# Kernel tuning notes

Measured on AMD Instinct MI355X. Metric: run time of the kernel, lower is better.

## Reference

```python
import jax, jax.numpy as jnp
import numpy as np

N_NODES = 40000
FEAT = 128
HID = 128
EMB = 64
N_EDGES = 640000


def setup_inputs() -> dict:
    key = jax.random.key(0)
    ks = jax.random.split(key, 8)
    x = jax.random.normal(ks[0], (N_NODES, FEAT), dtype=jnp.float32)
    edge_index = jax.random.randint(ks[1], (2, N_EDGES), 0, N_NODES, dtype=jnp.int64)
    s1 = 1.0 / np.sqrt(FEAT)
    s2 = 1.0 / np.sqrt(HID)
    W1_l = jax.random.uniform(ks[2], (HID, FEAT), jnp.float32, -s1, s1)
    b1 = jax.random.uniform(ks[3], (HID,), jnp.float32, -s1, s1)
    W1_r = jax.random.uniform(ks[4], (HID, FEAT), jnp.float32, -s1, s1)
    W2_l = jax.random.uniform(ks[5], (EMB, HID), jnp.float32, -s2, s2)
    b2 = jax.random.uniform(ks[6], (EMB,), jnp.float32, -s2, s2)
    W2_r = jax.random.uniform(ks[7], (EMB, HID), jnp.float32, -s2, s2)
    return {"x": x, "edge_index": edge_index, "W1_l": W1_l, "b1": b1,
            "W1_r": W1_r, "W2_l": W2_l, "b2": b2, "W2_r": W2_r}


def _sage_conv(x, src, dst, W_l, b_l, W_r, n_nodes):
    # mean aggregation of source-node features onto destination nodes
    msg = x[src]                                           # [E, d]
    agg = jax.ops.segment_sum(msg, dst, num_segments=n_nodes)   # [N, d]
    cnt = jax.ops.segment_sum(jnp.ones((src.shape[0],), x.dtype), dst,
                              num_segments=n_nodes)        # [N]
    agg = agg / jnp.maximum(cnt, 1.0)[:, None]
    # out = lin_l(mean_j x_j) + lin_r(x_i); bias lives in lin_l
    return agg @ W_l.T + b_l + x @ W_r.T


def reference(x, edge_index, W1_l, b1, W1_r, W2_l, b2, W2_r):
    src, dst = edge_index[0], edge_index[1]
    n = x.shape[0]
    h = _sage_conv(x, src, dst, W1_l, b1, W1_r, n)
    h = jax.nn.elu(h)
    # dropout p=0.2 is identity in eval mode
    h = _sage_conv(h, src, dst, W2_l, b2, W2_r, n)
    return jax.nn.log_softmax(h, axis=1)
```

## Files before the change

kernel.cpp:

```cpp
#include <hip/hip_runtime.h>
#include <hip/hip_fp16.h>
#include <math.h>

#define N_NODES 40000
#define FEATD 128
#define EMB 64
#define N_EDGES 640000
#define CAP 64

typedef unsigned short u16;
typedef __attribute__((ext_vector_type(8))) unsigned short u16x8;
typedef __attribute__((ext_vector_type(8))) _Float16 f16x8;
typedef __attribute__((ext_vector_type(4))) float f32x4;

__device__ __forceinline__ float h2f(u16 h) {
  __half hh;
  *(u16*)&hh = h;
  return __half2float(hh);
}
__device__ __forceinline__ u16 f2h(float f) {
  __half hh = __float2half(f);
  return *(u16*)&hh;
}

__global__ __launch_bounds__(256) void prep_kernel(
    const float* __restrict__ x, const float* __restrict__ W1l,
    const float* __restrict__ W1r, const float* __restrict__ W2l,
    const float* __restrict__ W2r, u16* __restrict__ xh,
    u16* __restrict__ wp) {
  int bid = blockIdx.x;
  if (bid < 2500) {
    int i = bid * 256 + threadIdx.x;
    float4 v0 = *(const float4*)(&x[i * 8]);
    float4 v1 = *(const float4*)(&x[i * 8 + 4]);
    u16x8 o;
    o[0] = f2h(v0.x); o[1] = f2h(v0.y); o[2] = f2h(v0.z); o[3] = f2h(v0.w);
    o[4] = f2h(v1.x); o[5] = f2h(v1.y); o[6] = f2h(v1.z); o[7] = f2h(v1.w);
    *(u16x8*)(&xh[i * 8]) = o;
  } else {
    int i = (bid - 2500) * 256 + threadIdx.x;
    const float* srcp;
    int off;
    if (i < 16384)      { srcp = W1l; off = i; }
    else if (i < 32768) { srcp = W1r; off = i - 16384; }
    else if (i < 40960) { srcp = W2l; off = i - 32768; }
    else                { srcp = W2r; off = i - 40960; }
    wp[i] = f2h(srcp[off]);
  }
}

__global__ __launch_bounds__(256) void fill_kernel(
    const int* __restrict__ src, const int* __restrict__ dst,
    int* __restrict__ deg, u16* __restrict__ bucket) {
  int e = blockIdx.x * 256 + threadIdx.x;
  if (e >= N_EDGES) return;
  int s = src[e];
  int d = dst[e];
  int pos = atomicAdd(&deg[d], 1);
  if (pos < CAP) bucket[d * CAP + pos] = (u16)s;
}

__global__ __launch_bounds__(256) void gather_mean_f16(
    const u16* __restrict__ xh, const int* __restrict__ deg,
    const u16* __restrict__ bucket, u16* __restrict__ aggh) {
  int n = blockIdx.x * 4 + (threadIdx.x >> 6);
  int lane = threadIdx.x & 63;
  int g = lane >> 4;
  int li = lane & 15;
  int dgf = deg[n];
  int dg = dgf < CAP ? dgf : CAP;
  float inv = 1.0f / fmaxf((float)dgf, 1.0f);
  const u16* bk = bucket + n * CAP;
  float acc[8];
#pragma unroll
  for (int i = 0; i < 8; i++) acc[i] = 0.f;
  for (int d = g; d < dg; d += 4) {
    u16x8 v = *(const u16x8*)(&xh[(int)bk[d] * 128 + li * 8]);
#pragma unroll
    for (int i = 0; i < 8; i++) acc[i] += h2f(v[i]);
  }
#pragma unroll
  for (int i = 0; i < 8; i++) {
    acc[i] += __shfl_xor(acc[i], 16);
    acc[i] += __shfl_xor(acc[i], 32);
  }
  if (g == 0) {
    u16x8 o;
#pragma unroll
    for (int i = 0; i < 8; i++) o[i] = f2h(acc[i] * inv);
    *(u16x8*)(&aggh[n * 128 + li * 8]) = o;
  }
}

__global__ __launch_bounds__(256) void gemm12_kernel(
    const u16* __restrict__ AggH, const u16* __restrict__ XH,
    const u16* __restrict__ wp, const float* __restrict__ b1v,
    const float* __restrict__ b2v, u16* __restrict__ Yh,
    float* __restrict__ Z) {
  const u16* w1l = wp;
  const u16* w1r = wp + 16384;
  const u16* w2l = wp + 32768;
  const u16* w2r = wp + 40960;

  __shared__ __align__(16) union {
    struct {
      u16 wl[128][72], wr[128][72];
      u16 a[64][72], x[64][72];
    } p1;
    struct {
      u16 h[64][136];
      u16 w2l[64][136], w2r[64][136];
    } p2;
  } L;

  const int tid = threadIdx.x;
  const int wv = tid >> 6;
  const int lane = tid & 63;
  const int li = lane & 15;
  const int q = lane >> 4;
  const int nbase = blockIdx.x * 64;

  f32x4 acc1[8];
#pragma unroll
  for (int jt = 0; jt < 8; jt++) acc1[jt] = (f32x4){0.f, 0.f, 0.f, 0.f};

  for (int kb = 0; kb < 2; kb++) {
#pragma unroll
    for (int it = 0; it < 4; it++) {
      int idx = tid + 256 * it;
      int j = idx >> 3, c = idx & 7;
      int go = j * 128 + kb * 64 + c * 8;
      *(u16x8*)(&L.p1.wl[j][c * 8]) = *(const u16x8*)(&w1l[go]);
      *(u16x8*)(&L.p1.wr[j][c * 8]) = *(const u16x8*)(&w1r[go]);
    }
#pragma unroll
    for (int it = 0; it < 2; it++) {
      int idx = tid + 256 * it;
      int n = idx >> 3, c = idx & 7;
      int go = (nbase + n) * 128 + kb * 64 + c * 8;
      *(u16x8*)(&L.p1.a[n][c * 8]) = *(const u16x8*)(&AggH[go]);
      *(u16x8*)(&L.p1.x[n][c * 8]) = *(const u16x8*)(&XH[go]);
    }
    __syncthreads();
#pragma unroll
    for (int kk = 0; kk < 2; kk++) {
      f16x8 aF = *(const f16x8*)(&L.p1.a[wv * 16 + li][kk * 32 + q * 8]);
      f16x8 xF = *(const f16x8*)(&L.p1.x[wv * 16 + li][kk * 32 + q * 8]);
#pragma unroll
      for (int jt = 0; jt < 8; jt++) {
        f16x8 wlF = *(const f16x8*)(&L.p1.wl[jt * 16 + li][kk * 32 + q * 8]);
        f16x8 wrF = *(const f16x8*)(&L.p1.wr[jt * 16 + li][kk * 32 + q * 8]);
        acc1[jt] = __builtin_amdgcn_mfma_f32_16x16x32_f16(aF, wlF, acc1[jt], 0, 0, 0);
        acc1[jt] = __builtin_amdgcn_mfma_f32_16x16x32_f16(xF, wrF, acc1[jt], 0, 0, 0);
      }
    }
    __syncthreads();
  }

#pragma unroll
  for (int jt = 0; jt < 8; jt++) {
    int j = jt * 16 + li;
    float bb = b1v[j];
#pragma unroll
    for (int r = 0; r < 4; r++) {
      float v = acc1[jt][r] + bb;
      v = v > 0.f ? v : expm1f(v);
      L.p2.h[wv * 16 + q * 4 + r][j] = f2h(v);
    }
  }
#pragma unroll
  for (int it = 0; it < 4; it++) {
    int idx = tid + 256 * it;
    int j = idx >> 4, c = idx & 15;
    int go = j * 128 + c * 8;
    *(u16x8*)(&L.p2.w2l[j][c * 8]) = *(const u16x8*)(&w2l[go]);
    *(u16x8*)(&L.p2.w2r[j][c * 8]) = *(const u16x8*)(&w2r[go]);
  }
  __syncthreads();

  f32x4 accY[4], accZ[4];
#pragma unroll
  for (int mt = 0; mt < 4; mt++) {
    accY[mt] = (f32x4){0.f, 0.f, 0.f, 0.f};
    accZ[mt] = (f32x4){0.f, 0.f, 0.f, 0.f};
  }
#pragma unroll
  for (int kc = 0; kc < 4; kc++) {
    f16x8 blF = *(const f16x8*)(&L.p2.w2l[wv * 16 + li][kc * 32 + q * 8]);
    f16x8 brF = *(const f16x8*)(&L.p2.w2r[wv * 16 + li][kc * 32 + q * 8]);
#pragma unroll
    for (int mt = 0; mt < 4; mt++) {
      f16x8 hF = *(const f16x8*)(&L.p2.h[mt * 16 + li][kc * 32 + q * 8]);
      accY[mt] = __builtin_amdgcn_mfma_f32_16x16x32_f16(hF, blF, accY[mt], 0, 0, 0);
      accZ[mt] = __builtin_amdgcn_mfma_f32_16x16x32_f16(hF, brF, accZ[mt], 0, 0, 0);
    }
  }

  {
    int j2 = wv * 16 + li;
    float bb = b2v[j2];
#pragma unroll
    for (int mt = 0; mt < 4; mt++) {
#pragma unroll
      for (int r = 0; r < 4; r++) {
        int node = nbase + mt * 16 + q * 4 + r;
        Yh[node * 64 + j2] = f2h(accY[mt][r]);
        Z[node * 64 + j2] = accZ[mt][r] + bb;
      }
    }
  }
}

__global__ __launch_bounds__(256) void final_kernel(
    const u16* __restrict__ Y, const float* __restrict__ Z,
    const int* __restrict__ deg, const u16* __restrict__ bucket,
    float* __restrict__ out) {
  int n = blockIdx.x * 4 + (threadIdx.x >> 6);
  int lane = threadIdx.x & 63;
  int g = lane >> 4;
  int li = lane & 15;
  int dgf = deg[n];
  int dg = dgf < CAP ? dgf : CAP;
  float inv = 1.0f / fmaxf((float)dgf, 1.0f);
  const u16* bk = bucket + n * CAP;
  float4 acc = {0.f, 0.f, 0.f, 0.f};
  for (int d = g; d < dg; d += 4) {
    ushort4 v = *(const ushort4*)(&Y[(int)bk[d] * 64 + li * 4]);
    acc.x += h2f(v.x); acc.y += h2f(v.y); acc.z += h2f(v.z); acc.w += h2f(v.w);
  }
  acc.x += __shfl_xor(acc.x, 16); acc.y += __shfl_xor(acc.y, 16);
  acc.z += __shfl_xor(acc.z, 16); acc.w += __shfl_xor(acc.w, 16);
  acc.x += __shfl_xor(acc.x, 32); acc.y += __shfl_xor(acc.y, 32);
  acc.z += __shfl_xor(acc.z, 32); acc.w += __shfl_xor(acc.w, 32);
  float4 zb = *(const float4*)(&Z[n * 64 + li * 4]);
  float4 v;
  v.x = zb.x + acc.x * inv; v.y = zb.y + acc.y * inv;
  v.z = zb.z + acc.z * inv; v.w = zb.w + acc.w * inv;
  float m = fmaxf(fmaxf(v.x, v.y), fmaxf(v.z, v.w));
  m = fmaxf(m, __shfl_xor(m, 1)); m = fmaxf(m, __shfl_xor(m, 2));
  m = fmaxf(m, __shfl_xor(m, 4)); m = fmaxf(m, __shfl_xor(m, 8));
  float s = __expf(v.x - m) + __expf(v.y - m) + __expf(v.z - m) + __expf(v.w - m);
  s += __shfl_xor(s, 1); s += __shfl_xor(s, 2);
  s += __shfl_xor(s, 4); s += __shfl_xor(s, 8);
  float lg = m + logf(s);
  if (lane < 16) {
    float4 o = {v.x - lg, v.y - lg, v.z - lg, v.w - lg};
    *(float4*)(&out[n * 64 + li * 4]) = o;
  }
}

extern "C" void kernel_launch(void* const* d_in, const int* in_sizes, int n_in,
                              void* d_out, int out_size, void* d_ws, size_t ws_size,
                              hipStream_t stream) {
  const float* x   = (const float*)d_in[0];
  const int*   ei  = (const int*)d_in[1];
  const float* W1l = (const float*)d_in[2];
  const float* b1  = (const float*)d_in[3];
  const float* W1r = (const float*)d_in[4];
  const float* W2l = (const float*)d_in[5];
  const float* b2  = (const float*)d_in[6];
  const float* W2r = (const float*)d_in[7];
  float* out = (float*)d_out;

  const int* src = ei;
  const int* dst = ei + N_EDGES;

  u16* bucket = (u16*)d_ws;
  int* deg = (int*)(bucket + (size_t)N_NODES * CAP);
  u16* xh = (u16*)(deg + N_NODES);
  u16* aggh = xh + (size_t)N_NODES * FEATD;
  u16* yh = aggh + (size_t)N_NODES * FEATD;
  float* z = (float*)(yh + (size_t)N_NODES * EMB);
  u16* wp = (u16*)(z + (size_t)N_NODES * EMB);

  hipMemsetAsync(deg, 0, N_NODES * sizeof(int), stream);
  prep_kernel<<<2500 + 192, 256, 0, stream>>>(x, W1l, W1r, W2l, W2r, xh, wp);
  fill_kernel<<<(N_EDGES + 255) / 256, 256, 0, stream>>>(src, dst, deg, bucket);

  gather_mean_f16<<<N_NODES / 4, 256, 0, stream>>>(xh, deg, bucket, aggh);
  gemm12_kernel<<<N_NODES / 64, 256, 0, stream>>>(aggh, xh, wp, b1, b2, yh, z);
  final_kernel<<<N_NODES / 4, 256, 0, stream>>>(yh, z, deg, bucket, out);
}
```

Measured before the change: 193.8 us.

## Fuse neighbor gather into GEMM kernel and merge prep with edge fill

Merges the edge-bucket fill into the fp16 conversion kernel, and folds the layer-1 mean aggregation into the GEMM kernel: each thread gathers a quarter row of a node's neighbors into shared memory, and the weight and x fragments are read directly from global memory instead of being staged. This removes two launches and the aggh round trip through global memory. Z is now stored in fp16. The risks are a serialized per-thread gather with 32 accumulators (register pressure, less memory parallelism), uncoalesced direct global weight loads, fp16 precision loss in Z, and fill running concurrently with prep in the same launch.

```diff
diff --git a/kernel.cpp b/kernel.cpp
--- a/kernel.cpp
+++ b/kernel.cpp
@@ -23,11 +23,12 @@
   return *(u16*)&hh;
 }
 
-__global__ __launch_bounds__(256) void prep_kernel(
+__global__ __launch_bounds__(256) void prep_fill_kernel(
     const float* __restrict__ x, const float* __restrict__ W1l,
     const float* __restrict__ W1r, const float* __restrict__ W2l,
-    const float* __restrict__ W2r, u16* __restrict__ xh,
-    u16* __restrict__ wp) {
+    const float* __restrict__ W2r, const int* __restrict__ src,
+    const int* __restrict__ dst, u16* __restrict__ xh,
+    u16* __restrict__ wp, int* __restrict__ deg, u16* __restrict__ bucket) {
   int bid = blockIdx.x;
   if (bid < 2500) {
     int i = bid * 256 + threadIdx.x;
@@ -37,7 +38,7 @@
     o[0] = f2h(v0.x); o[1] = f2h(v0.y); o[2] = f2h(v0.z); o[3] = f2h(v0.w);
     o[4] = f2h(v1.x); o[5] = f2h(v1.y); o[6] = f2h(v1.z); o[7] = f2h(v1.w);
     *(u16x8*)(&xh[i * 8]) = o;
-  } else {
+  } else if (bid < 2692) {
     int i = (bid - 2500) * 256 + threadIdx.x;
     const float* srcp;
     int off;
@@ -46,72 +47,28 @@
     else if (i < 40960) { srcp = W2l; off = i - 32768; }
     else                { srcp = W2r; off = i - 40960; }
     wp[i] = f2h(srcp[off]);
-  }
-}
-
-__global__ __launch_bounds__(256) void fill_kernel(
-    const int* __restrict__ src, const int* __restrict__ dst,
-    int* __restrict__ deg, u16* __restrict__ bucket) {
-  int e = blockIdx.x * 256 + threadIdx.x;
-  if (e >= N_EDGES) return;
-  int s = src[e];
-  int d = dst[e];
-  int pos = atomicAdd(&deg[d], 1);
-  if (pos < CAP) bucket[d * CAP + pos] = (u16)s;
-}
-
-__global__ __launch_bounds__(256) void gather_mean_f16(
-    const u16* __restrict__ xh, const int* __restrict__ deg,
-    const u16* __restrict__ bucket, u16* __restrict__ aggh) {
-  int n = blockIdx.x * 4 + (threadIdx.x >> 6);
-  int lane = threadIdx.x & 63;
-  int g = lane >> 4;
-  int li = lane & 15;
-  int dgf = deg[n];
-  int dg = dgf < CAP ? dgf : CAP;
-  float inv = 1.0f / fmaxf((float)dgf, 1.0f);
-  const u16* bk = bucket + n * CAP;
-  float acc[8];
-#pragma unroll
-  for (int i = 0; i < 8; i++) acc[i] = 0.f;
-  for (int d = g; d < dg; d += 4) {
-    u16x8 v = *(const u16x8*)(&xh[(int)bk[d] * 128 + li * 8]);
-#pragma unroll
-    for (int i = 0; i < 8; i++) acc[i] += h2f(v[i]);
-  }
-#pragma unroll
-  for (int i = 0; i < 8; i++) {
-    acc[i] += __shfl_xor(acc[i], 16);
-    acc[i] += __shfl_xor(acc[i], 32);
-  }
-  if (g == 0) {
-    u16x8 o;
-#pragma unroll
-    for (int i = 0; i < 8; i++) o[i] = f2h(acc[i] * inv);
-    *(u16x8*)(&aggh[n * 128 + li * 8]) = o;
+  } else {
+    int e = (bid - 2692) * 256 + threadIdx.x;
+    if (e >= N_EDGES) return;
+    int s = src[e];
+    int d = dst[e];
+    int pos = atomicAdd(&deg[d], 1);
+    if (pos < CAP) bucket[d * CAP + pos] = (u16)s;
   }
 }
 
 __global__ __launch_bounds__(256) void gemm12_kernel(
-    const u16* __restrict__ AggH, const u16* __restrict__ XH,
-    const u16* __restrict__ wp, const float* __restrict__ b1v,
-    const float* __restrict__ b2v, u16* __restrict__ Yh,
-    float* __restrict__ Z) {
+    const u16* __restrict__ xh, const u16* __restrict__ wp,
+    const float* __restrict__ b1v, const float* __restrict__ b2v,
+    const int* __restrict__ deg, const u16* __restrict__ bucket,
+    u16* __restrict__ Yh, u16* __restrict__ Zh) {
   const u16* w1l = wp;
   const u16* w1r = wp + 16384;
   const u16* w2l = wp + 32768;
   const u16* w2r = wp + 40960;
 
-  __shared__ __align__(16) union {
-    struct {
-      u16 wl[128][72], wr[128][72];
-      u16 a[64][72], x[64][72];
-    } p1;
-    struct {
-      u16 h[64][136];
-      u16 w2l[64][136], w2r[64][136];
-    } p2;
-  } L;
+  __shared__ __align__(16) u16 sAgg[64][136];
+  __shared__ __align__(16) u16 sH[64][136];
 
   const int tid = threadIdx.x;
   const int wv = tid >> 6;
@@ -120,41 +77,56 @@
   const int q = lane >> 4;
   const int nbase = blockIdx.x * 64;
 
+  {
+    int n = tid >> 2;
+    int g = tid & 3;
+    int gn = nbase + n;
+    int dgf = deg[gn];
+    int dg = dgf < CAP ? dgf : CAP;
+    float inv = 1.0f / fmaxf((float)dgf, 1.0f);
+    const u16* bk = bucket + gn * CAP;
+    float acc[32];
+#pragma unroll
+    for (int i = 0; i < 32; i++) acc[i] = 0.f;
+    for (int d = 0; d < dg; d++) {
+      const u16* row = &xh[(int)bk[d] * 128 + g * 32];
+      u16x8 v0 = *(const u16x8*)(row);
+      u16x8 v1 = *(const u16x8*)(row + 8);
+      u16x8 v2 = *(const u16x8*)(row + 16);
+      u16x8 v3 = *(const u16x8*)(row + 24);
+#pragma unroll
+      for (int i = 0; i < 8; i++) {
+        acc[i]      += h2f(v0[i]);
+        acc[8 + i]  += h2f(v1[i]);
+        acc[16 + i] += h2f(v2[i]);
+        acc[24 + i] += h2f(v3[i]);
+      }
+    }
+#pragma unroll
+    for (int c = 0; c < 4; c++) {
+      u16x8 o;
+#pragma unroll
+      for (int i = 0; i < 8; i++) o[i] = f2h(acc[c * 8 + i] * inv);
+      *(u16x8*)(&sAgg[n][g * 32 + c * 8]) = o;
+    }
+  }
+  __syncthreads();
+
   f32x4 acc1[8];
 #pragma unroll
   for (int jt = 0; jt < 8; jt++) acc1[jt] = (f32x4){0.f, 0.f, 0.f, 0.f};
 
-  for (int kb = 0; kb < 2; kb++) {
-#pragma unroll
-    for (int it = 0; it < 4; it++) {
-      int idx = tid + 256 * it;
-      int j = idx >> 3, c = idx & 7;
-      int go = j * 128 + kb * 64 + c * 8;
-      *(u16x8*)(&L.p1.wl[j][c * 8]) = *(const u16x8*)(&w1l[go]);
-      *(u16x8*)(&L.p1.wr[j][c * 8]) = *(const u16x8*)(&w1r[go]);
-    }
-#pragma unroll
-    for (int it = 0; it < 2; it++) {
-      int idx = tid + 256 * it;
-      int n = idx >> 3, c = idx & 7;
-      int go = (nbase + n) * 128 + kb * 64 + c * 8;
-      *(u16x8*)(&L.p1.a[n][c * 8]) = *(const u16x8*)(&AggH[go]);
-      *(u16x8*)(&L.p1.x[n][c * 8]) = *(const u16x8*)(&XH[go]);
-    }
-    __syncthreads();
-#pragma unroll
-    for (int kk = 0; kk < 2; kk++) {
-      f16x8 aF = *(const f16x8*)(&L.p1.a[wv * 16 + li][kk * 32 + q * 8]);
-      f16x8 xF = *(const f16x8*)(&L.p1.x[wv * 16 + li][kk * 32 + q * 8]);
-#pragma unroll
-      for (int jt = 0; jt < 8; jt++) {
-        f16x8 wlF = *(const f16x8*)(&L.p1.wl[jt * 16 + li][kk * 32 + q * 8]);
-        f16x8 wrF = *(const f16x8*)(&L.p1.wr[jt * 16 + li][kk * 32 + q * 8]);
-        acc1[jt] = __builtin_amdgcn_mfma_f32_16x16x32_f16(aF, wlF, acc1[jt], 0, 0, 0);
-        acc1[jt] = __builtin_amdgcn_mfma_f32_16x16x32_f16(xF, wrF, acc1[jt], 0, 0, 0);
-      }
-    }
-    __syncthreads();
+#pragma unroll
+  for (int kc = 0; kc < 4; kc++) {
+    f16x8 aF = *(const f16x8*)(&sAgg[wv * 16 + li][kc * 32 + q * 8]);
+    f16x8 xF = *(const f16x8*)(&xh[(nbase + wv * 16 + li) * 128 + kc * 32 + q * 8]);
+#pragma unroll
+    for (int jt = 0; jt < 8; jt++) {
+      f16x8 wlF = *(const f16x8*)(&w1l[(jt * 16 + li) * 128 + kc * 32 + q * 8]);
+      f16x8 wrF = *(const f16x8*)(&w1r[(jt * 16 + li) * 128 + kc * 32 + q * 8]);
+      acc1[jt] = __builtin_amdgcn_mfma_f32_16x16x32_f16(aF, wlF, acc1[jt], 0, 0, 0);
+      acc1[jt] = __builtin_amdgcn_mfma_f32_16x16x32_f16(xF, wrF, acc1[jt], 0, 0, 0);
+    }
   }
 
 #pragma unroll
@@ -165,16 +137,8 @@
     for (int r = 0; r < 4; r++) {
       float v = acc1[jt][r] + bb;
       v = v > 0.f ? v : expm1f(v);
-      L.p2.h[wv * 16 + q * 4 + r][j] = f2h(v);
-    }
-  }
-#pragma unroll
-  for (int it = 0; it < 4; it++) {
-    int idx = tid + 256 * it;
-    int j = idx >> 4, c = idx & 15;
-    int go = j * 128 + c * 8;
-    *(u16x8*)(&L.p2.w2l[j][c * 8]) = *(const u16x8*)(&w2l[go]);
-    *(u16x8*)(&L.p2.w2r[j][c * 8]) = *(const u16x8*)(&w2r[go]);
+      sH[wv * 16 + q * 4 + r][j] = f2h(v);
+    }
   }
   __syncthreads();
 
@@ -186,11 +150,11 @@
   }
 #pragma unroll
   for (int kc = 0; kc < 4; kc++) {
-    f16x8 blF = *(const f16x8*)(&L.p2.w2l[wv * 16 + li][kc * 32 + q * 8]);
-    f16x8 brF = *(const f16x8*)(&L.p2.w2r[wv * 16 + li][kc * 32 + q * 8]);
+    f16x8 blF = *(const f16x8*)(&w2l[(wv * 16 + li) * 128 + kc * 32 + q * 8]);
+    f16x8 brF = *(const f16x8*)(&w2r[(wv * 16 + li) * 128 + kc * 32 + q * 8]);
 #pragma unroll
     for (int mt = 0; mt < 4; mt++) {
-      f16x8 hF = *(const f16x8*)(&L.p2.h[mt * 16 + li][kc * 32 + q * 8]);
+      f16x8 hF = *(const f16x8*)(&sH[mt * 16 + li][kc * 32 + q * 8]);
       accY[mt] = __builtin_amdgcn_mfma_f32_16x16x32_f16(hF, blF, accY[mt], 0, 0, 0);
       accZ[mt] = __builtin_amdgcn_mfma_f32_16x16x32_f16(hF, brF, accZ[mt], 0, 0, 0);
     }
@@ -205,14 +169,14 @@
       for (int r = 0; r < 4; r++) {
         int node = nbase + mt * 16 + q * 4 + r;
         Yh[node * 64 + j2] = f2h(accY[mt][r]);
-        Z[node * 64 + j2] = accZ[mt][r] + bb;
+        Zh[node * 64 + j2] = f2h(accZ[mt][r] + bb);
       }
     }
   }
 }
 
 __global__ __launch_bounds__(256) void final_kernel(
-    const u16* __restrict__ Y, const float* __restrict__ Z,
+    const u16* __restrict__ Y, const u16* __restrict__ Z,
     const int* __restrict__ deg, const u16* __restrict__ bucket,
     float* __restrict__ out) {
   int n = blockIdx.x * 4 + (threadIdx.x >> 6);
@@ -232,10 +196,10 @@
   acc.z += __shfl_xor(acc.z, 16); acc.w += __shfl_xor(acc.w, 16);
   acc.x += __shfl_xor(acc.x, 32); acc.y += __shfl_xor(acc.y, 32);
   acc.z += __shfl_xor(acc.z, 32); acc.w += __shfl_xor(acc.w, 32);
-  float4 zb = *(const float4*)(&Z[n * 64 + li * 4]);
+  ushort4 zb4 = *(const ushort4*)(&Z[n * 64 + li * 4]);
   float4 v;
-  v.x = zb.x + acc.x * inv; v.y = zb.y + acc.y * inv;
-  v.z = zb.z + acc.z * inv; v.w = zb.w + acc.w * inv;
+  v.x = h2f(zb4.x) + acc.x * inv; v.y = h2f(zb4.y) + acc.y * inv;
+  v.z = h2f(zb4.z) + acc.z * inv; v.w = h2f(zb4.w) + acc.w * inv;
   float m = fmaxf(fmaxf(v.x, v.y), fmaxf(v.z, v.w));
   m = fmaxf(m, __shfl_xor(m, 1)); m = fmaxf(m, __shfl_xor(m, 2));
   m = fmaxf(m, __shfl_xor(m, 4)); m = fmaxf(m, __shfl_xor(m, 8));
@@ -268,16 +232,13 @@
   u16* bucket = (u16*)d_ws;
   int* deg = (int*)(bucket + (size_t)N_NODES * CAP);
   u16* xh = (u16*)(deg + N_NODES);
-  u16* aggh = xh + (size_t)N_NODES * FEATD;
-  u16* yh = aggh + (size_t)N_NODES * FEATD;
-  float* z = (float*)(yh + (size_t)N_NODES * EMB);
-  u16* wp = (u16*)(z + (size_t)N_NODES * EMB);
+  u16* yh = xh + (size_t)N_NODES * FEATD;
+  u16* zh = yh + (size_t)N_NODES * EMB;
+  u16* wp = zh + (size_t)N_NODES * EMB;
 
   hipMemsetAsync(deg, 0, N_NODES * sizeof(int), stream);
-  prep_kernel<<<2500 + 192, 256, 0, stream>>>(x, W1l, W1r, W2l, W2r, xh, wp);
-  fill_kernel<<<(N_EDGES + 255) / 256, 256, 0, stream>>>(src, dst, deg, bucket);
-
-  gather_mean_f16<<<N_NODES / 4, 256, 0, stream>>>(xh, deg, bucket, aggh);
-  gemm12_kernel<<<N_NODES / 64, 256, 0, stream>>>(aggh, xh, wp, b1, b2, yh, z);
-  final_kernel<<<N_NODES / 4, 256, 0, stream>>>(yh, z, deg, bucket, out);
-}
+  prep_fill_kernel<<<2500 + 192 + 2500, 256, 0, stream>>>(
+      x, W1l, W1r, W2l, W2r, src, dst, xh, wp, deg, bucket);
+  gemm12_kernel<<<N_NODES / 64, 256, 0, stream>>>(xh, wp, b1, b2, deg, bucket, yh, zh);
+  final_kernel<<<N_NODES / 4, 256, 0, stream>>>(yh, zh, deg, bucket, out);
+}
```

New measurement: 216.5 us. +11.7%, slower.
